# Performance work log

Measured on AMD Instinct MI355X. Metric: run time of the kernel, lower is better.

Reference implementation:

```python
import jax, jax.numpy as jnp
import numpy as np

# Hardcoded non-tensor forward args (kernels_desc / kernels_radius / input dims):
# kernels_desc = [{'weight': 1.0, 'xy': 6.0, 'image': 0.1}], kernels_radius = [3, 3, 3]
# height_input = width_input = depth_input = prediction resolution (pool is identity).
R0, R1 = 3, 3
WEIGHT = 1.0
SIGMA_XY = 6.0
SIGMA_IMG = 0.1


def _unfold(img, r0, r1):
    # torch unfoldNd equivalent: (N, C, kh, kw, H*W), zero padding, stride 1.
    N, C, H, W = img.shape
    p = jnp.pad(img, ((0, 0), (0, 0), (r0, r0), (r1, r1)))
    shifts = [p[:, :, i:i + H, j:j + W]
              for i in range(2 * r0 + 1) for j in range(2 * r1 + 1)]
    out = jnp.stack(shifts, axis=2)  # (N, C, kh*kw, H, W)
    return out.reshape(N, C, 2 * r0 + 1, 2 * r1 + 1, H * W)


def _forward(y_hat_softmax, sample):
    N, C, H, W, D = y_hat_softmax.shape
    Ci = sample.shape[1]
    NB = N * D
    # fold depth into batch: (N*D, C, H, W)
    y = y_hat_softmax.transpose(0, 4, 1, 2, 3).reshape(NB, C, H, W)
    s = sample.transpose(0, 4, 1, 2, 3).reshape(NB, Ci, H, W)
    # adaptive_avg_pool2d to (H, W): input res == pred res here -> identity.
    # xy mesh features (row index channel, then col index channel)
    rows = jnp.broadcast_to(jnp.arange(H, dtype=y.dtype)[None, None, :, None], (NB, 1, H, W))
    cols = jnp.broadcast_to(jnp.arange(W, dtype=y.dtype)[None, None, None, :], (NB, 1, H, W))
    feats = jnp.concatenate([rows / SIGMA_XY, cols / SIGMA_XY, s / SIGMA_IMG], axis=1)
    # Gaussian affinity kernel over local windows
    fu = _unfold(feats, R0, R1)                         # (NB, Cf, kh, kw, HW)
    center = fu[:, :, R0, R1, :][:, :, None, None, :]
    k = WEIGHT * jnp.exp(-0.5 * ((fu - center) ** 2).sum(axis=1, keepdims=True))
    k = k.at[:, :, R0, R1, :].set(0.0)                  # zero self-affinity
    # weighted sum of neighbor predictions
    yu = _unfold(y, R0, R1)                             # (NB, C, kh, kw, HW)
    kh_kw = (2 * R0 + 1) * (2 * R1 + 1)
    prod = (k * yu).reshape(NB, C, kh_kw, H * W).sum(axis=2).reshape(NB, C, H, W)
    loss = k.sum() - (prod * y).sum()
    denom = NB * H * W
    return loss / denom


def setup_inputs() -> dict:
    key = jax.random.key(0)
    k1, k2 = jax.random.split(key)
    N, C, H, W, D = 2, 2, 64, 64, 64
    logits = jax.random.normal(k1, (N, C, H, W, D), dtype=jnp.float32)
    y = jax.nn.softmax(logits, axis=1)  # prediction must be a softmax over channels
    sample = jax.random.normal(k2, (N, 1, H, W, D), dtype=jnp.float32)
    return {"y_hat_softmax": y, "sample": sample}


def reference(y_hat_softmax, sample):
    return _forward(y_hat_softmax, sample)
```

## Files before the change

kernel.cpp:

```cpp
#include <hip/hip_runtime.h>


constexpr int N = 2, H = 64, W = 64, D = 64, R = 3;
constexpr int WD  = W * D;
constexpr int HWD = H * W * D;
constexpr float INV_SXY  = 1.0f / 6.0f;
constexpr float LOG2E    = 1.4426950408889634f;
constexpr float C2       = 50.0f * LOG2E;
constexpr int GBLOCKS = N * H * (W / 16);
constexpr int NBLOCKS = 4 * GBLOCKS;

__device__ __forceinline__ float exp2_fast(float x) {
    return __builtin_amdgcn_exp2f(x);
}

template <int DI0, int DJ0, int DI1, int DJ1, int DI2, int DJ2,
          int DI3, int DJ3, int DI4, int DJ4, int DI5, int DJ5>
__device__ __forceinline__ float group_sum(
    const float* __restrict__ sb, const float* __restrict__ y0b,
    int cidx, int h, int w,
    const float scv[4], const float bv[4]) {
    constexpr int DI[6] = {DI0, DI1, DI2, DI3, DI4, DI5};
    constexpr int DJ[6] = {DJ0, DJ1, DJ2, DJ3, DJ4, DJ5};

    bool   vld[6];
    float4 sn[6], an[6];

    #pragma unroll
    for (int p = 0; p < 6; ++p) {
        const bool v = ((unsigned)(h + DI[p]) < (unsigned)H) &
                       ((unsigned)(w + DJ[p]) < (unsigned)W);
        vld[p] = v;
        const int off = v ? (DI[p] * WD + DJ[p] * D) : 0;
        sn[p] = *(const float4*)(sb  + cidx + off);
        an[p] = *(const float4*)(y0b + cidx + off);
    }

    float acc = 0.0f;
    #pragma unroll
    for (int p = 0; p < 6; ++p) {
        constexpr float d2[6] = {
            (float)(DI0 * DI0 + DJ0 * DJ0), (float)(DI1 * DI1 + DJ1 * DJ1),
            (float)(DI2 * DI2 + DJ2 * DJ2), (float)(DI3 * DI3 + DJ3 * DJ3),
            (float)(DI4 * DI4 + DJ4 * DJ4), (float)(DI5 * DI5 + DJ5 * DJ5)};
        const float A2  = -0.5f * d2[p] * (INV_SXY * INV_SXY) * LOG2E;
        const float A2e = vld[p] ? A2 : -1e30f;
        const float snv[4] = {sn[p].x, sn[p].y, sn[p].z, sn[p].w};
        const float anv[4] = {an[p].x, an[p].y, an[p].z, an[p].w};
        #pragma unroll
        for (int j = 0; j < 4; ++j) {
            const float dsr = snv[j] - scv[j];
            const float k   = exp2_fast(__builtin_fmaf(-C2 * dsr, dsr, A2e));
            const float ab  = anv[j] * bv[j];
            acc += k * (anv[j] + bv[j] - 2.0f * ab);
        }
    }
    return acc;
}

__global__ __launch_bounds__(256) void crf_partial(
    const float* __restrict__ y,
    const float* __restrict__ s,
    float* __restrict__ partial) {
    const int tid   = threadIdx.x;
    const int d0    = (tid & 15) << 2;
    const int wlane = tid >> 4;
    const int bid   = blockIdx.x;
    const int sbid  = bid & (GBLOCKS - 1);
    const int g     = bid >> 9;
    const int w = ((sbid & 3) << 4) + wlane;
    const int h = (sbid >> 2) & 63;
    const int n = sbid >> 8;

    const float* sb  = s + (size_t)n * HWD;
    const float* y0b = y + (size_t)n * (2 * HWD);

    const int cidx = h * WD + w * D + d0;
    const float4 sc4 = *(const float4*)(sb  + cidx);
    const float4 b4  = *(const float4*)(y0b + cidx);
    const float scv[4] = {sc4.x, sc4.y, sc4.z, sc4.w};
    const float bv[4]  = {b4.x,  b4.y,  b4.z,  b4.w};

    float acc = 0.0f;
    float extra = 0.0f;
    if (g == 0) {
        acc = group_sum<0, 1, 0, 2, 0, 3, 1, -3, 1, -2, 1, -1>(
            sb, y0b, cidx, h, w, scv, bv);
        const int nrows = min(h + R, H - 1) - max(h - R, 0) + 1;
        const int ncols = min(w + R, W - 1) - max(w - R, 0) + 1;
        const int oob = 49 - nrows * ncols;
        if (oob) {
            const float fh = (float)h * INV_SXY;
            const float fw = (float)w * INV_SXY;
            const float base2 = -0.5f * (fh * fh + fw * fw) * LOG2E;
            float koob = 0.0f;
            #pragma unroll
            for (int j = 0; j < 4; ++j)
                koob += exp2_fast(__builtin_fmaf(-C2 * scv[j], scv[j], base2));
            extra = (float)oob * koob;
        }
    } else if (g == 1) {
        acc = group_sum<1, 0, 1, 1, 1, 2, 1, 3, 2, -3, 2, -2>(
            sb, y0b, cidx, h, w, scv, bv);
    } else if (g == 2) {
        acc = group_sum<2, -1, 2, 0, 2, 1, 2, 2, 2, 3, 3, -3>(
            sb, y0b, cidx, h, w, scv, bv);
    } else {
        acc = group_sum<3, -2, 3, -1, 3, 0, 3, 1, 3, 2, 3, 3>(
            sb, y0b, cidx, h, w, scv, bv);
    }

    float part = 2.0f * acc + extra;

    #pragma unroll
    for (int off = 32; off; off >>= 1)
        part += __shfl_down(part, off, 64);

    __shared__ float wsum[4];
    if ((tid & 63) == 0) wsum[tid >> 6] = part;
    __syncthreads();
    if (tid == 0) partial[bid] = wsum[0] + wsum[1] + wsum[2] + wsum[3];
}

__global__ __launch_bounds__(256) void reduce_partials(
    const float* __restrict__ partial, float* __restrict__ out) {
    const int tid = threadIdx.x;
    float v = 0.0f;
    #pragma unroll
    for (int i = 0; i < NBLOCKS / 256; ++i)
        v += partial[tid + i * 256];
    #pragma unroll
    for (int off = 32; off; off >>= 1)
        v += __shfl_down(v, off, 64);
    __shared__ float wsum[4];
    if ((tid & 63) == 0) wsum[tid >> 6] = v;
    __syncthreads();
    if (tid == 0)
        out[0] = (wsum[0] + wsum[1] + wsum[2] + wsum[3]) *
                 (1.0f / (float)(N * D * H * W));
}

extern "C" void kernel_launch(void* const* d_in, const int* in_sizes, int n_in,
                              void* d_out, int out_size, void* d_ws, size_t ws_size,
                              hipStream_t stream) {
    const float* y = (const float*)d_in[0];
    const float* s = (const float*)d_in[1];
    float* partial = (float*)d_ws;

    crf_partial<<<dim3(NBLOCKS), dim3(256), 0, stream>>>(y, s, partial);
    reduce_partials<<<dim3(1), dim3(256), 0, stream>>>(partial, (float*)d_out);
}
```

Measured before the change: 62.69 us.

## Stage input row tiles in LDS and compute all neighbor groups per block

Each block now loads four image rows (h..h+3) for a 16-wide depth slice of s and y into shared memory. All 24 half-window neighbor offsets are then evaluated from LDS, where before four separate block groups each re-read their neighbors from global memory. The block-to-row mapping is arranged so each XCD gets a contiguous band of rows, which should help L2 reuse of overlapping halo rows. The block count drops from 2048 to 512, so occupancy and parallelism are lower and each thread does four times the exp work.

After: 62.20 us. About the same (-0.8%).

```diff
diff --git a/kernel.cpp b/kernel.cpp
--- a/kernel.cpp
+++ b/kernel.cpp
@@ -7,8 +7,7 @@
 constexpr float INV_SXY  = 1.0f / 6.0f;
 constexpr float LOG2E    = 1.4426950408889634f;
 constexpr float C2       = 50.0f * LOG2E;
-constexpr int GBLOCKS = N * H * (W / 16);
-constexpr int NBLOCKS = 4 * GBLOCKS;
+constexpr int NBLOCKS = 2 * 64 * 4;
 
 __device__ __forceinline__ float exp2_fast(float x) {
     return __builtin_amdgcn_exp2f(x);
@@ -16,10 +15,9 @@
 
 template <int DI0, int DJ0, int DI1, int DJ1, int DI2, int DJ2,
           int DI3, int DJ3, int DI4, int DJ4, int DI5, int DJ5>
-__device__ __forceinline__ float group_sum(
-    const float* __restrict__ sb, const float* __restrict__ y0b,
-    int cidx, int h, int w,
-    const float scv[4], const float bv[4]) {
+__device__ __forceinline__ float group_sum_lds(
+    const float* __restrict__ sT, const float* __restrict__ yT,
+    int w, int doff, int h, const float scv[4], const float bv[4]) {
     constexpr int DI[6] = {DI0, DI1, DI2, DI3, DI4, DI5};
     constexpr int DJ[6] = {DJ0, DJ1, DJ2, DJ3, DJ4, DJ5};
 
@@ -28,12 +26,12 @@
 
     #pragma unroll
     for (int p = 0; p < 6; ++p) {
-        const bool v = ((unsigned)(h + DI[p]) < (unsigned)H) &
-                       ((unsigned)(w + DJ[p]) < (unsigned)W);
-        vld[p] = v;
-        const int off = v ? (DI[p] * WD + DJ[p] * D) : 0;
-        sn[p] = *(const float4*)(sb  + cidx + off);
-        an[p] = *(const float4*)(y0b + cidx + off);
+        vld[p] = (h + DI[p] < H) &
+                 ((unsigned)(w + DJ[p]) < (unsigned)W);
+        const int wcl = min(max(w + DJ[p], 0), W - 1);
+        const int off = (DI[p] * W + wcl) * 16 + doff;
+        sn[p] = *(const float4*)(sT + off);
+        an[p] = *(const float4*)(yT + off);
     }
 
     float acc = 0.0f;
@@ -62,30 +60,54 @@
     const float* __restrict__ y,
     const float* __restrict__ s,
     float* __restrict__ partial) {
-    const int tid   = threadIdx.x;
-    const int d0    = (tid & 15) << 2;
-    const int wlane = tid >> 4;
-    const int bid   = blockIdx.x;
-    const int sbid  = bid & (GBLOCKS - 1);
-    const int g     = bid >> 9;
-    const int w = ((sbid & 3) << 4) + wlane;
-    const int h = (sbid >> 2) & 63;
-    const int n = sbid >> 8;
+    const int tid = threadIdx.x;
+    const int bid = blockIdx.x;
+
+    const int xcd = bid & 7;
+    const int q   = bid >> 3;
+    const int h   = (xcd << 3) | (q & 7);
+    const int dq  = (q >> 3) & 3;
+    const int n   = q >> 5;
+    const int pidx = ((n << 6) + h) * 4 + dq;
+    const int d0b  = dq << 4;
 
     const float* sb  = s + (size_t)n * HWD;
     const float* y0b = y + (size_t)n * (2 * HWD);
 
-    const int cidx = h * WD + w * D + d0;
-    const float4 sc4 = *(const float4*)(sb  + cidx);
-    const float4 b4  = *(const float4*)(y0b + cidx);
+    __shared__ float sT[4 * 64 * 16];
+    __shared__ float yT[4 * 64 * 16];
+    #pragma unroll
+    for (int c = 0; c < 4; ++c) {
+        const int fidx = (c << 10) + (tid << 2);
+        const int wg   = (fidx >> 4) & 63;
+        const int dd   = fidx & 15;
+        const int hh   = min(h + c, H - 1);
+        const int gidx = hh * WD + wg * D + d0b + dd;
+        *(float4*)(sT + fidx) = *(const float4*)(sb  + gidx);
+        *(float4*)(yT + fidx) = *(const float4*)(y0b + gidx);
+    }
+    __syncthreads();
+
+    const int w    = tid >> 2;
+    const int doff = (tid & 3) << 2;
+
+    const float4 sc4 = *(const float4*)(sT + w * 16 + doff);
+    const float4 b4  = *(const float4*)(yT + w * 16 + doff);
     const float scv[4] = {sc4.x, sc4.y, sc4.z, sc4.w};
     const float bv[4]  = {b4.x,  b4.y,  b4.z,  b4.w};
 
     float acc = 0.0f;
+    acc += group_sum_lds<0, 1, 0, 2, 0, 3, 1, -3, 1, -2, 1, -1>(
+        sT, yT, w, doff, h, scv, bv);
+    acc += group_sum_lds<1, 0, 1, 1, 1, 2, 1, 3, 2, -3, 2, -2>(
+        sT, yT, w, doff, h, scv, bv);
+    acc += group_sum_lds<2, -1, 2, 0, 2, 1, 2, 2, 2, 3, 3, -3>(
+        sT, yT, w, doff, h, scv, bv);
+    acc += group_sum_lds<3, -2, 3, -1, 3, 0, 3, 1, 3, 2, 3, 3>(
+        sT, yT, w, doff, h, scv, bv);
+
     float extra = 0.0f;
-    if (g == 0) {
-        acc = group_sum<0, 1, 0, 2, 0, 3, 1, -3, 1, -2, 1, -1>(
-            sb, y0b, cidx, h, w, scv, bv);
+    {
         const int nrows = min(h + R, H - 1) - max(h - R, 0) + 1;
         const int ncols = min(w + R, W - 1) - max(w - R, 0) + 1;
         const int oob = 49 - nrows * ncols;
@@ -99,15 +121,6 @@
                 koob += exp2_fast(__builtin_fmaf(-C2 * scv[j], scv[j], base2));
             extra = (float)oob * koob;
         }
-    } else if (g == 1) {
-        acc = group_sum<1, 0, 1, 1, 1, 2, 1, 3, 2, -3, 2, -2>(
-            sb, y0b, cidx, h, w, scv, bv);
-    } else if (g == 2) {
-        acc = group_sum<2, -1, 2, 0, 2, 1, 2, 2, 2, 3, 3, -3>(
-            sb, y0b, cidx, h, w, scv, bv);
-    } else {
-        acc = group_sum<3, -2, 3, -1, 3, 0, 3, 1, 3, 2, 3, 3>(
-            sb, y0b, cidx, h, w, scv, bv);
     }
 
     float part = 2.0f * acc + extra;
@@ -119,7 +132,7 @@
     __shared__ float wsum[4];
     if ((tid & 63) == 0) wsum[tid >> 6] = part;
     __syncthreads();
-    if (tid == 0) partial[bid] = wsum[0] + wsum[1] + wsum[2] + wsum[3];
+    if (tid == 0) partial[pidx] = wsum[0] + wsum[1] + wsum[2] + wsum[3];
 }
 
 __global__ __launch_bounds__(256) void reduce_partials(
```
